# Kernel tuning notes

Hardware: AMD Instinct MI355X
Metric: run time of the kernel (lower is better)

## Reference

```python
import jax, jax.numpy as jnp
import numpy as np

D = 1024      # model dimension
H = 16        # heads
DK = D // H   # head dim
DFF = 4096    # ffn hidden
B, S = 2, 2048
EPS = 1e-6
NEG_SLOPE = 0.01  # torch LeakyReLU default


def setup_inputs() -> dict:
    key = jax.random.key(0)
    ks = jax.random.split(key, 12)
    sd = 1.0 / np.sqrt(D)
    sf = 1.0 / np.sqrt(DFF)
    return {
        "x": jax.random.normal(ks[0], (B, S, D), dtype=jnp.float32),
        "wq": jax.random.uniform(ks[1], (D, D), jnp.float32, -sd, sd),
        "bq": jnp.zeros((D,), jnp.float32),
        "wk": jax.random.uniform(ks[2], (D, D), jnp.float32, -sd, sd),
        "bk": jnp.zeros((D,), jnp.float32),
        "wv": jax.random.uniform(ks[3], (D, D), jnp.float32, -sd, sd),
        "bv": jnp.zeros((D,), jnp.float32),
        "wo": jax.random.uniform(ks[4], (D, D), jnp.float32, -sd, sd),
        "bo": jnp.zeros((D,), jnp.float32),
        "g1": jnp.ones((D,), jnp.float32),
        "b1": jnp.zeros((D,), jnp.float32),
        "w_ff1": jax.random.uniform(ks[5], (D, DFF), jnp.float32, -sd, sd),
        "b_ff1": jnp.zeros((DFF,), jnp.float32),
        "w_ff2": jax.random.uniform(ks[6], (DFF, D), jnp.float32, -sf, sf),
        "b_ff2": jnp.zeros((D,), jnp.float32),
        "g2": jnp.ones((D,), jnp.float32),
        "b2": jnp.zeros((D,), jnp.float32),
    }


def _layernorm(x, g, b):
    mu = jnp.mean(x, axis=-1, keepdims=True)
    var = jnp.mean(jnp.square(x - mu), axis=-1, keepdims=True)
    return (x - mu) * jax.lax.rsqrt(var + EPS) * g + b


def reference(x, wq, bq, wk, bk, wv, bv, wo, bo, g1, b1,
              w_ff1, b_ff1, w_ff2, b_ff2, g2, b2):
    # Multi-head attention
    q = (x @ wq + bq).reshape(B, S, H, DK).transpose(0, 2, 1, 3)  # [B,H,S,DK]
    k = (x @ wk + bk).reshape(B, S, H, DK).transpose(0, 2, 1, 3)
    v = (x @ wv + bv).reshape(B, S, H, DK).transpose(0, 2, 1, 3)
    scores = jnp.einsum('bhqd,bhkd->bhqk', q, k) / np.sqrt(DK)
    attn = jax.nn.softmax(scores, axis=-1)
    ctx = jnp.einsum('bhqk,bhkd->bhqd', attn, v)
    ctx = ctx.transpose(0, 2, 1, 3).reshape(B, S, D)
    attn_out = ctx @ wo + bo
    # residual + LN1 (dropout = identity in eval)
    h = _layernorm(attn_out + x, g1, b1)
    # FFN with LeakyReLU
    ff = jnp.where(h @ w_ff1 + b_ff1 > 0,
                   h @ w_ff1 + b_ff1,
                   NEG_SLOPE * (h @ w_ff1 + b_ff1))
    ff = ff @ w_ff2 + b_ff2
    return _layernorm(ff + h, g2, b2)
```

## Files before the change

### kernel.cpp

```cpp
#include <hip/hip_runtime.h>
#include <math.h>

#define D_MODEL 1024
#define NHEAD   16
#define DKH     64
#define DFF_    4096
#define BB      2
#define SS      2048
#define MTOT    (BB*SS)
#define EPSLN   1e-6f
#define NEG_SLOPE 0.01f

typedef unsigned short u16;
typedef unsigned int   u32;
typedef __bf16 bf16x8 __attribute__((ext_vector_type(8)));
typedef float  f32x4  __attribute__((ext_vector_type(4)));
typedef u16    u16x4  __attribute__((ext_vector_type(4)));

__device__ __forceinline__ u16 f2bf(float f) {
    u32 u = __float_as_uint(f);
    u = (u + 0x7fffu + ((u >> 16) & 1u)) >> 16;
    return (u16)u;
}
__device__ __forceinline__ float bf2f(u16 u) {
    return __uint_as_float(((u32)u) << 16);
}

__device__ __forceinline__ void gload_lds16(const u16* g, u16* l) {
    __builtin_amdgcn_global_load_lds(
        (const __attribute__((address_space(1))) u32*)g,
        (__attribute__((address_space(3))) u32*)l,
        16, 0, 0);
}

__device__ __forceinline__ void transpose_tile(const float* __restrict__ W,
        u16* __restrict__ WT, int N, int out_stride, int out_row_off,
        float scale, int bx, int by, u16* T)
{
    const int t  = threadIdx.x;
    const int n0 = bx * 64;
    const int k0 = by * 64;
    #pragma unroll
    for (int i = 0; i < 4; ++i) {
        int r = i * 16 + (t >> 4);
        int c = (t & 15) * 4;
        float4 v = *(const float4*)&W[(size_t)(k0 + r) * N + n0 + c];
        T[(c + 0) * 72 + r] = f2bf(v.x * scale);
        T[(c + 1) * 72 + r] = f2bf(v.y * scale);
        T[(c + 2) * 72 + r] = f2bf(v.z * scale);
        T[(c + 3) * 72 + r] = f2bf(v.w * scale);
    }
    __syncthreads();
    #pragma unroll
    for (int i = 0; i < 4; ++i) {
        int nr = i * 16 + (t >> 4);
        int kc = (t & 15) * 4;
        u16x4 o = { T[nr*72 + kc], T[nr*72 + kc + 1], T[nr*72 + kc + 2], T[nr*72 + kc + 3] };
        *(u16x4*)&WT[(size_t)(out_row_off + n0 + nr) * out_stride + k0 + kc] = o;
    }
}

__global__ __launch_bounds__(256)
void prep(const float* __restrict__ x, u16* __restrict__ x_bf,
          const float* __restrict__ wq, const float* __restrict__ wk,
          const float* __restrict__ wv, const float* __restrict__ wo,
          const float* __restrict__ wff1, const float* __restrict__ wff2,
          u16* __restrict__ wqkvT, u16* __restrict__ woT,
          u16* __restrict__ wff1T, u16* __restrict__ wff2T,
          const float* __restrict__ bq, const float* __restrict__ bk,
          const float* __restrict__ bv, float* __restrict__ qkv_bias,
          float qscale)
{
    __shared__ u16 T[64 * 72];
    int blk = blockIdx.x;
    if (blk < 4096) {
        int i = blk * 256 + threadIdx.x;
        float4 v = ((const float4*)x)[i];
        u16x4 o = { f2bf(v.x), f2bf(v.y), f2bf(v.z), f2bf(v.w) };
        ((u16x4*)x_bf)[i] = o;
        return;
    }
    blk -= 4096;
    if (blk < 1024) {
        int which = blk >> 8, r = blk & 255;
        const float* Ws = which == 0 ? wq : which == 1 ? wk : which == 2 ? wv : wo;
        u16* Wd   = which == 3 ? woT : wqkvT;
        int off   = which == 3 ? 0 : which * 1024;
        float sc  = which == 0 ? qscale : 1.0f;
        transpose_tile(Ws, Wd, 1024, 1024, off, sc, r & 15, r >> 4, T);
        return;
    }
    blk -= 1024;
    if (blk < 1024) {
        transpose_tile(wff1, wff1T, 4096, 1024, 0, 1.0f, blk & 63, blk >> 6, T);
        return;
    }
    blk -= 1024;
    if (blk < 1024) {
        transpose_tile(wff2, wff2T, 1024, 4096, 0, 1.0f, blk & 15, blk >> 4, T);
        return;
    }
    blk -= 1024;
    int i = blk * 256 + threadIdx.x;
    qkv_bias[i] = (i < 1024) ? bq[i] * qscale
                : (i < 2048) ? bk[i - 1024] : bv[i - 2048];
}

template<int EPI>
__global__ __launch_bounds__(256)
void gemm_bf16(const u16* __restrict__ A, const u16* __restrict__ BT,
               const float* __restrict__ bias, void* __restrict__ Cout,
               u16* __restrict__ Vt, int M, int N, int k_len, int kstride)
{
    __shared__ u16 As[128 * 64];
    __shared__ u16 Bs[128 * 64];
    const int tid  = threadIdx.x;
    const int w    = tid >> 6;
    const int lane = tid & 63;
    const int lm   = lane & 15;
    const int lq   = lane >> 4;
    const int nf = gridDim.x * gridDim.y;
    int f = blockIdx.y * gridDim.x + blockIdx.x;
    f = (f & 7) * (nf >> 3) + (f >> 3);
    const int row0 = (f / gridDim.x) * 128;
    const int col0 = (f % gridDim.x) * 128;
    const int k_off = blockIdx.z * k_len;
    const int wrow = (w >> 1) * 64;
    const int wcol = (w & 1) * 64;

    f32x4 acc[4][4] = {};

    const int r_i = lane >> 3;
    const int csw = ((lane & 7) ^ r_i) * 8;
    const u16* a_src = A  + (size_t)(row0 + w * 32 + r_i) * kstride + k_off + csw;
    const u16* b_src = BT + (size_t)(col0 + w * 32 + r_i) * kstride + k_off + csw;
    u16* a_dst = &As[(w * 32) * 64];
    u16* b_dst = &Bs[(w * 32) * 64];

    const int fr0 = (lq ^ (lm & 7)) * 8;
    const int fr1 = ((4 + lq) ^ (lm & 7)) * 8;
    const u16* a_rd = &As[(wrow + lm) * 64];
    const u16* b_rd = &Bs[(wcol + lm) * 64];

    for (int k0 = 0; k0 < k_len; k0 += 64) {
        #pragma unroll
        for (int i = 0; i < 4; ++i) {
            gload_lds16(a_src + k0 + (size_t)(i * 8) * kstride, a_dst + (i * 8) * 64);
            gload_lds16(b_src + k0 + (size_t)(i * 8) * kstride, b_dst + (i * 8) * 64);
        }
        __syncthreads();
        #pragma unroll
        for (int h = 0; h < 2; ++h) {
            const int fo = h ? fr1 : fr0;
            bf16x8 av[4], bv[4];
            #pragma unroll
            for (int m = 0; m < 4; ++m) av[m] = *(const bf16x8*)(a_rd + m * 16 * 64 + fo);
            #pragma unroll
            for (int n = 0; n < 4; ++n) bv[n] = *(const bf16x8*)(b_rd + n * 16 * 64 + fo);
            #pragma unroll
            for (int m = 0; m < 4; ++m)
                #pragma unroll
                for (int n = 0; n < 4; ++n)
                    acc[m][n] = __builtin_amdgcn_mfma_f32_16x16x32_bf16(av[m], bv[n], acc[m][n], 0, 0, 0);
        }
        __syncthreads();
    }

    float bz[4] = {0.f, 0.f, 0.f, 0.f};
    if (EPI != 3) {
        #pragma unroll
        for (int n = 0; n < 4; ++n) bz[n] = bias[col0 + wcol + n * 16 + lm];
    }

    if (EPI == 4 && col0 >= 2048) {
        #pragma unroll
        for (int m = 0; m < 4; ++m) {
            int rbase = row0 + wrow + m * 16 + lq * 4;
            int b = rbase >> 11, s = rbase & 2047;
            #pragma unroll
            for (int n = 0; n < 4; ++n) {
                int c = col0 + wcol + n * 16 + lm - 2048;
                u16x4 pk = { f2bf(acc[m][n][0] + bz[n]), f2bf(acc[m][n][1] + bz[n]),
                             f2bf(acc[m][n][2] + bz[n]), f2bf(acc[m][n][3] + bz[n]) };
                *(u16x4*)&Vt[(size_t)((b * 16 + (c >> 6)) * 64 + (c & 63)) * 2048 + s] = pk;
            }
        }
        return;
    }

    u16* Cz = (u16*)Cout + (EPI == 3 ? (size_t)blockIdx.z * M * N : 0);
    #pragma unroll
    for (int m = 0; m < 4; ++m) {
        #pragma unroll
        for (int e = 0; e < 4; ++e) {
            int row = row0 + wrow + m * 16 + lq * 4 + e;
            #pragma unroll
            for (int n = 0; n < 4; ++n) {
                int col = col0 + wcol + n * 16 + lm;
                float v = acc[m][n][e] + bz[n];
                if (EPI == 1) v = v > 0.f ? v : NEG_SLOPE * v;
                Cz[(size_t)row * N + col] = f2bf(v);
            }
        }
    }
}

__global__ __launch_bounds__(256, 4)
void attn_mfma(const u16* __restrict__ QKV, const u16* __restrict__ Vt,
               u16* __restrict__ ctx)
{
    __shared__ u16 QP[64 * 64];
    __shared__ u16 Kb[2][64 * 64];
    __shared__ u16 Vb[2][64 * 64];
    const int tid = threadIdx.x, w = tid >> 6, lane = tid & 63;
    const int lm = lane & 15, lq = lane >> 4;
    const int qh = w >> 1;
    const int kh = w & 1;
    int f = blockIdx.y * 32 + blockIdx.x;
    f = (f & 7) * 128 + (f >> 3);
    const int q0 = (f & 31) * 64;
    const int bh = f >> 5;
    const int b  = bh >> 4, h = bh & 15;
    const size_t row_b = (size_t)b * SS;
    const int ccol = h * DKH;

    const int r_i = lane >> 3;
    const int csw = ((lane & 7) ^ r_i) * 8;
    const u16* ksrc = QKV + (row_b + w * 16 + r_i) * 3072 + 1024 + ccol + csw;
    const u16* vsrc = Vt + ((size_t)bh * 64 + w * 16 + r_i) * SS + csw;
    const u16* qsrc = QKV + (row_b + q0 + w * 16 + r_i) * 3072 + ccol + csw;

    gload_lds16(qsrc,                    &QP[(w * 16) * 64]);
    gload_lds16(qsrc + (size_t)8 * 3072, &QP[(w * 16 + 8) * 64]);
    #pragma unroll
    for (int i = 0; i < 2; ++i) {
        gload_lds16(ksrc + (size_t)(i * 8) * 3072, &Kb[0][(w * 16 + i * 8) * 64]);
        gload_lds16(vsrc + (size_t)(i * 8) * SS,   &Vb[0][(w * 16 + i * 8) * 64]);
    }
    __syncthreads();

    const int fr0 = (lq ^ (lm & 7)) * 8;
    const int fr1 = ((4 + lq) ^ (lm & 7)) * 8;
    const int frp = kh ? fr1 : fr0;

    bf16x8 aq[2][2];
    #pragma unroll
    for (int m = 0; m < 2; ++m) {
        aq[m][0] = *(const bf16x8*)&QP[(qh * 32 + m * 16 + lm) * 64 + fr0];
        aq[m][1] = *(const bf16x8*)&QP[(qh * 32 + m * 16 + lm) * 64 + fr1];
    }
    __syncthreads();

    bf16x8 ones;
    #pragma unroll
    for (int j = 0; j < 8; ++j) ones[j] = (__bf16)1.0f;

    f32x4 o[2][4] = {};
    f32x4 lacc[2] = {};

    for (int kt = 0; kt < SS / 64; ++kt) {
        const int cur = kt & 1;
        if (kt < SS / 64 - 1) {
            const int nxt = cur ^ 1;
            const size_t koff = (size_t)(kt + 1) * 64;
            #pragma unroll
            for (int i = 0; i < 2; ++i) {
                gload_lds16(ksrc + (koff + i * 8) * 3072, &Kb[nxt][(w * 16 + i * 8) * 64]);
                gload_lds16(vsrc + koff + (size_t)(i * 8) * SS, &Vb[nxt][(w * 16 + i * 8) * 64]);
            }
        }
        f32x4 s[2][2] = {};
        #pragma unroll
        for (int n = 0; n < 2; ++n) {
            bf16x8 bk0 = *(const bf16x8*)&Kb[cur][(kh * 32 + n * 16 + lm) * 64 + fr0];
            bf16x8 bk1 = *(const bf16x8*)&Kb[cur][(kh * 32 + n * 16 + lm) * 64 + fr1];
            #pragma unroll
            for (int m = 0; m < 2; ++m) {
                s[m][n] = __builtin_amdgcn_mfma_f32_16x16x32_bf16(aq[m][0], bk0, s[m][n], 0, 0, 0);
                s[m][n] = __builtin_amdgcn_mfma_f32_16x16x32_bf16(aq[m][1], bk1, s[m][n], 0, 0, 0);
            }
        }
        const int rb = lq * 4;
        const int cw = lm & 7;
        #pragma unroll
        for (int m = 0; m < 2; ++m) {
            #pragma unroll
            for (int n = 0; n < 2; ++n) {
                const int cb = kh * 4 + n * 2 + (lm >> 3);
                #pragma unroll
                for (int e = 0; e < 4; ++e) {
                    float p = __builtin_exp2f(s[m][n][e]);
                    const int row = qh * 32 + m * 16 + rb + e;
                    QP[row * 64 + ((cb ^ ((rb + e) & 7)) * 8) + cw] =
                        (u16)((__float_as_uint(p) + 0x8000u) >> 16);
                }
            }
        }
        bf16x8 ap[2];
        #pragma unroll
        for (int m = 0; m < 2; ++m)
            ap[m] = *(const bf16x8*)&QP[(qh * 32 + m * 16 + lm) * 64 + frp];
        #pragma unroll
        for (int n = 0; n < 4; ++n) {
            bf16x8 bv = *(const bf16x8*)&Vb[cur][(n * 16 + lm) * 64 + frp];
            #pragma unroll
            for (int m = 0; m < 2; ++m)
                o[m][n] = __builtin_amdgcn_mfma_f32_16x16x32_bf16(ap[m], bv, o[m][n], 0, 0, 0);
        }
        #pragma unroll
        for (int m = 0; m < 2; ++m)
            lacc[m] = __builtin_amdgcn_mfma_f32_16x16x32_bf16(ap[m], ones, lacc[m], 0, 0, 0);
        __syncthreads();
    }

    if (kh == 1) {
        float* red = (float*)(qh == 0 ? (void*)Kb : (void*)Vb);
        #pragma unroll
        for (int m = 0; m < 2; ++m) {
            #pragma unroll
            for (int n = 0; n < 4; ++n)
                #pragma unroll
                for (int e = 0; e < 4; ++e)
                    red[((m * 4 + n) * 4 + e) * 64 + lane] = o[m][n][e];
            #pragma unroll
            for (int e = 0; e < 4; ++e)
                red[(32 + m * 4 + e) * 64 + lane] = lacc[m][e];
        }
    }
    __syncthreads();
    if (kh == 0) {
        const float* red = (const float*)(qh == 0 ? (void*)Kb : (void*)Vb);
        #pragma unroll
        for (int m = 0; m < 2; ++m) {
            #pragma unroll
            for (int e = 0; e < 4; ++e)
                lacc[m][e] += red[(32 + m * 4 + e) * 64 + lane];
            #pragma unroll
            for (int e = 0; e < 4; ++e) {
                float inv = 1.0f / lacc[m][e];
                int row = q0 + qh * 32 + m * 16 + lq * 4 + e;
                u16* dst = ctx + (row_b + row) * D_MODEL + ccol;
                #pragma unroll
                for (int n = 0; n < 4; ++n) {
                    float v = o[m][n][e] + red[((m * 4 + n) * 4 + e) * 64 + lane];
                    dst[n * 16 + lm] = f2bf(v * inv);
                }
            }
        }
    }
}

template<int OUTF32, int RESBF>
__global__ __launch_bounds__(256)
void add_ln(const u16* __restrict__ C0, const u16* __restrict__ C1,
            const float* __restrict__ cbias, const void* __restrict__ resid,
            const float* __restrict__ g, const float* __restrict__ beta,
            float* __restrict__ outf, u16* __restrict__ outb)
{
    __shared__ float red[8];
    const int row = blockIdx.x;
    const int tid = threadIdx.x;
    u16x4 p0 = ((const u16x4*)(C0 + (size_t)row * D_MODEL))[tid];
    u16x4 p1 = ((const u16x4*)(C1 + (size_t)row * D_MODEL))[tid];
    float4 cb = ((const float4*)cbias)[tid];
    float4 rr;
    if (RESBF) {
        u16x4 rb = ((const u16x4*)((const u16*)resid + (size_t)row * D_MODEL))[tid];
        rr = { bf2f(rb.x), bf2f(rb.y), bf2f(rb.z), bf2f(rb.w) };
    } else {
        rr = ((const float4*)((const float*)resid + (size_t)row * D_MODEL))[tid];
    }
    float4 v = { bf2f(p0.x) + bf2f(p1.x) + cb.x + rr.x,
                 bf2f(p0.y) + bf2f(p1.y) + cb.y + rr.y,
                 bf2f(p0.z) + bf2f(p1.z) + cb.z + rr.z,
                 bf2f(p0.w) + bf2f(p1.w) + cb.w + rr.w };
    float s  = v.x + v.y + v.z + v.w;
    float sq = v.x*v.x + v.y*v.y + v.z*v.z + v.w*v.w;
    #pragma unroll
    for (int off = 32; off > 0; off >>= 1) {
        s  += __shfl_down(s,  off, 64);
        sq += __shfl_down(sq, off, 64);
    }
    const int wv = tid >> 6;
    if ((tid & 63) == 0) { red[wv] = s; red[4 + wv] = sq; }
    __syncthreads();
    float st  = red[0] + red[1] + red[2] + red[3];
    float sqt = red[4] + red[5] + red[6] + red[7];
    float mu   = st * (1.0f / D_MODEL);
    float var  = sqt * (1.0f / D_MODEL) - mu * mu;
    float rstd = rsqrtf(var + EPSLN);
    float4 gv = ((const float4*)g)[tid];
    float4 bt = ((const float4*)beta)[tid];
    float4 ov;
    ov.x = (v.x - mu) * rstd * gv.x + bt.x;
    ov.y = (v.y - mu) * rstd * gv.y + bt.y;
    ov.z = (v.z - mu) * rstd * gv.z + bt.z;
    ov.w = (v.w - mu) * rstd * gv.w + bt.w;
    if (OUTF32) {
        ((float4*)(outf + (size_t)row * D_MODEL))[tid] = ov;
    } else {
        u16x4 ob = { f2bf(ov.x), f2bf(ov.y), f2bf(ov.z), f2bf(ov.w) };
        ((u16x4*)(outb + (size_t)row * D_MODEL))[tid] = ob;
    }
}

extern "C" void kernel_launch(void* const* d_in, const int* in_sizes, int n_in,
                              void* d_out, int out_size, void* d_ws, size_t ws_size,
                              hipStream_t stream) {
    const float* x     = (const float*)d_in[0];
    const float* wq    = (const float*)d_in[1];
    const float* bq    = (const float*)d_in[2];
    const float* wk    = (const float*)d_in[3];
    const float* bk    = (const float*)d_in[4];
    const float* wv    = (const float*)d_in[5];
    const float* bv    = (const float*)d_in[6];
    const float* wo    = (const float*)d_in[7];
    const float* bo    = (const float*)d_in[8];
    const float* g1    = (const float*)d_in[9];
    const float* b1    = (const float*)d_in[10];
    const float* w_ff1 = (const float*)d_in[11];
    const float* b_ff1 = (const float*)d_in[12];
    const float* w_ff2 = (const float*)d_in[13];
    const float* b_ff2 = (const float*)d_in[14];
    const float* g2    = (const float*)d_in[15];
    const float* b2    = (const float*)d_in[16];
    float* out = (float*)d_out;

    const float qscale = 0.18033688011112042f;

    char* W = (char*)d_ws;
    u16*   x_bf    = (u16*)(W + 0);
    u16*   wqkvT   = (u16*)(W + 8388608);
    u16*   woT     = (u16*)(W + 14680064);
    u16*   wff1T   = (u16*)(W + 16777216);
    u16*   wff2T   = (u16*)(W + 25165824);
    u16*   QKV     = (u16*)(W + 33554432);
    u16*   VtG     = (u16*)(W + 58720256);
    u16*   C0      = (u16*)(W + 67108864);
    u16*   C1      = (u16*)(W + 75497472);
    u16*   h_bf    = (u16*)(W + 83886080);
    float* qkv_bias= (float*)(W + 92274688);
    u16*   ctx     = x_bf;
    u16*   ff1_bf  = QKV;

    dim3 blk(256);
    prep<<<7180, blk, 0, stream>>>(x, x_bf, wq, wk, wv, wo, w_ff1, w_ff2,
                                   wqkvT, woT, wff1T, wff2T,
                                   bq, bk, bv, qkv_bias, qscale);
    gemm_bf16<4><<<dim3(24, 32, 1), blk, 0, stream>>>(x_bf, wqkvT, qkv_bias, QKV, VtG, MTOT, 3072, 1024, 1024);
    attn_mfma<<<dim3(32, 32), blk, 0, stream>>>(QKV, VtG, ctx);
    gemm_bf16<3><<<dim3(8, 32, 2), blk, 0, stream>>>(ctx, woT, nullptr, C0, nullptr, MTOT, 1024, 512, 1024);
    add_ln<0, 0><<<MTOT, blk, 0, stream>>>(C0, C1, bo, x, g1, b1, nullptr, h_bf);
    gemm_bf16<1><<<dim3(32, 32, 1), blk, 0, stream>>>(h_bf, wff1T, b_ff1, ff1_bf, nullptr, MTOT, DFF_, 1024, 1024);
    gemm_bf16<3><<<dim3(8, 32, 2), blk, 0, stream>>>(ff1_bf, wff2T, nullptr, C0, nullptr, MTOT, 1024, 2048, 4096);
    add_ln<1, 1><<<MTOT, blk, 0, stream>>>(C0, C1, b_ff2, h_bf, g2, b2, out, nullptr);
}
```

Measured before the change: 357.3 us.

## Add 256x256-tile 512-thread GEMM kernel for QKV and FFN1 projections

Adds a new GEMM kernel with 256x256 output tiles, 8 waves per block, double-buffered LDS with direct global-to-LDS loads interleaved between MFMA phases, and a grouped block-index swizzle for L2 locality. It replaces the 128-tile GEMM for the QKV and first FFN projections. The aim is more reuse per loaded operand and better overlap of loads with compute. The cost is 128KB of LDS per block and a large accumulator register footprint. The QKV grid of 192 blocks may leave some of the 256 CUs idle.

Measured after the change: 350.8 us. Within noise of the previous version (-1.8%).

```diff
diff --git a/kernel.cpp b/kernel.cpp
--- a/kernel.cpp
+++ b/kernel.cpp
@@ -172,14 +172,132 @@
         for (int n = 0; n < 4; ++n) bz[n] = bias[col0 + wcol + n * 16 + lm];
     }
 
+    u16* Cz = (u16*)Cout + (EPI == 3 ? (size_t)blockIdx.z * M * N : 0);
+    #pragma unroll
+    for (int m = 0; m < 4; ++m) {
+        #pragma unroll
+        for (int e = 0; e < 4; ++e) {
+            int row = row0 + wrow + m * 16 + lq * 4 + e;
+            #pragma unroll
+            for (int n = 0; n < 4; ++n) {
+                int col = col0 + wcol + n * 16 + lm;
+                float v = acc[m][n][e] + bz[n];
+                if (EPI == 1) v = v > 0.f ? v : NEG_SLOPE * v;
+                Cz[(size_t)row * N + col] = f2bf(v);
+            }
+        }
+    }
+}
+
+#define GPHASE(p) { \
+    bf16x8 a0h0 = *(const bf16x8*)&ar[(wm * 128 + (p) * 32 + lm) * 64 + fr0]; \
+    bf16x8 a0h1 = *(const bf16x8*)&ar[(wm * 128 + (p) * 32 + lm) * 64 + fr1]; \
+    bf16x8 a1h0 = *(const bf16x8*)&ar[(wm * 128 + (p) * 32 + 16 + lm) * 64 + fr0]; \
+    bf16x8 a1h1 = *(const bf16x8*)&ar[(wm * 128 + (p) * 32 + 16 + lm) * 64 + fr1]; \
+    _Pragma("unroll") \
+    for (int n = 0; n < 4; ++n) { \
+        acc[2*(p)][n]   = __builtin_amdgcn_mfma_f32_16x16x32_bf16(a0h0, bvf[n][0], acc[2*(p)][n], 0, 0, 0); \
+        acc[2*(p)][n]   = __builtin_amdgcn_mfma_f32_16x16x32_bf16(a0h1, bvf[n][1], acc[2*(p)][n], 0, 0, 0); \
+        acc[2*(p)+1][n] = __builtin_amdgcn_mfma_f32_16x16x32_bf16(a1h0, bvf[n][0], acc[2*(p)+1][n], 0, 0, 0); \
+        acc[2*(p)+1][n] = __builtin_amdgcn_mfma_f32_16x16x32_bf16(a1h1, bvf[n][1], acc[2*(p)+1][n], 0, 0, 0); \
+    } }
+
+template<int EPI>
+__global__ __launch_bounds__(512, 2)
+void gemm256(const u16* __restrict__ A, const u16* __restrict__ BT,
+             const float* __restrict__ bias, void* __restrict__ Cout,
+             u16* __restrict__ Vt, int M, int N, int k_len, int kstride)
+{
+    __shared__ u16 AS[2][256 * 64];
+    __shared__ u16 BS[2][256 * 64];
+    const int tid  = threadIdx.x;
+    const int w    = tid >> 6;
+    const int lane = tid & 63;
+    const int lm   = lane & 15;
+    const int lq   = lane >> 4;
+    const int wm   = w >> 2;
+    const int wn   = w & 3;
+
+    const int gx = gridDim.x;
+    const int nf = gx * gridDim.y;
+    int f = blockIdx.y * gx + blockIdx.x;
+    f = (f & 7) * (nf >> 3) + (f >> 3);
+    const int row0 = (f / gx) * 256;
+    const int col0 = (f % gx) * 256;
+
+    const int r_i = lane >> 3;
+    const int csw = ((lane & 7) ^ r_i) * 8;
+    const u16* a_src = A  + (size_t)(row0 + w * 8 + r_i) * kstride + csw;
+    const u16* b_src = BT + (size_t)(col0 + w * 8 + r_i) * kstride + csw;
+
+    const int fr0 = (lq ^ (lm & 7)) * 8;
+    const int fr1 = ((4 + lq) ^ (lm & 7)) * 8;
+
+    f32x4 acc[8][4] = {};
+    const int NT = k_len >> 6;
+
+    #pragma unroll
+    for (int j = 0; j < 4; ++j) {
+        gload_lds16(a_src + (size_t)(j * 64) * kstride, &AS[0][(j * 64 + w * 8) * 64]);
+        gload_lds16(b_src + (size_t)(j * 64) * kstride, &BS[0][(j * 64 + w * 8) * 64]);
+    }
+    __syncthreads();
+
+    for (int kt = 0; kt < NT; ++kt) {
+        const int cb = kt & 1, nb = cb ^ 1;
+        const bool pre = (kt + 1) < NT;
+        const u16* ar = &AS[cb][0];
+        const u16* br = &BS[cb][0];
+        u16* aw = &AS[nb][0];
+        u16* bw = &BS[nb][0];
+        const size_t knext = (size_t)(kt + 1) * 64;
+
+        if (pre) {
+            #pragma unroll
+            for (int j = 0; j < 4; ++j)
+                gload_lds16(b_src + (size_t)(j * 64) * kstride + knext,
+                            bw + (j * 64 + w * 8) * 64);
+            asm volatile("s_waitcnt vmcnt(6)" ::: "memory");
+        } else {
+            asm volatile("s_waitcnt vmcnt(2)" ::: "memory");
+        }
+        bf16x8 bvf[4][2];
+        #pragma unroll
+        for (int n = 0; n < 4; ++n) {
+            bvf[n][0] = *(const bf16x8*)&br[(wn * 64 + n * 16 + lm) * 64 + fr0];
+            bvf[n][1] = *(const bf16x8*)&br[(wn * 64 + n * 16 + lm) * 64 + fr1];
+        }
+        GPHASE(0)
+        if (pre) {
+            gload_lds16(a_src + knext,                                 aw + (w * 8) * 64);
+            gload_lds16(a_src + (size_t)128 * kstride + knext,         aw + (128 + w * 8) * 64);
+        }
+        GPHASE(1)
+        if (pre) {
+            gload_lds16(a_src + (size_t)64 * kstride + knext,          aw + (64 + w * 8) * 64);
+            gload_lds16(a_src + (size_t)192 * kstride + knext,         aw + (192 + w * 8) * 64);
+            asm volatile("s_waitcnt vmcnt(8)" ::: "memory");
+        } else {
+            asm volatile("s_waitcnt vmcnt(0)" ::: "memory");
+        }
+        GPHASE(2)
+        GPHASE(3)
+        asm volatile("" ::: "memory");
+        __builtin_amdgcn_s_barrier();
+    }
+
+    float bz[4];
+    #pragma unroll
+    for (int n = 0; n < 4; ++n) bz[n] = bias[col0 + wn * 64 + n * 16 + lm];
+
     if (EPI == 4 && col0 >= 2048) {
         #pragma unroll
-        for (int m = 0; m < 4; ++m) {
-            int rbase = row0 + wrow + m * 16 + lq * 4;
+        for (int m = 0; m < 8; ++m) {
+            int rbase = row0 + wm * 128 + m * 16 + lq * 4;
             int b = rbase >> 11, s = rbase & 2047;
             #pragma unroll
             for (int n = 0; n < 4; ++n) {
-                int c = col0 + wcol + n * 16 + lm - 2048;
+                int c = col0 + wn * 64 + n * 16 + lm - 2048;
                 u16x4 pk = { f2bf(acc[m][n][0] + bz[n]), f2bf(acc[m][n][1] + bz[n]),
                              f2bf(acc[m][n][2] + bz[n]), f2bf(acc[m][n][3] + bz[n]) };
                 *(u16x4*)&Vt[(size_t)((b * 16 + (c >> 6)) * 64 + (c & 63)) * 2048 + s] = pk;
@@ -188,15 +306,15 @@
         return;
     }
 
-    u16* Cz = (u16*)Cout + (EPI == 3 ? (size_t)blockIdx.z * M * N : 0);
-    #pragma unroll
-    for (int m = 0; m < 4; ++m) {
+    u16* Cz = (u16*)Cout;
+    #pragma unroll
+    for (int m = 0; m < 8; ++m) {
         #pragma unroll
         for (int e = 0; e < 4; ++e) {
-            int row = row0 + wrow + m * 16 + lq * 4 + e;
+            int row = row0 + wm * 128 + m * 16 + lq * 4 + e;
             #pragma unroll
             for (int n = 0; n < 4; ++n) {
-                int col = col0 + wcol + n * 16 + lm;
+                int col = col0 + wn * 64 + n * 16 + lm;
                 float v = acc[m][n][e] + bz[n];
                 if (EPI == 1) v = v > 0.f ? v : NEG_SLOPE * v;
                 Cz[(size_t)row * N + col] = f2bf(v);
@@ -444,14 +562,15 @@
     u16*   ff1_bf  = QKV;
 
     dim3 blk(256);
+    dim3 blk5(512);
     prep<<<7180, blk, 0, stream>>>(x, x_bf, wq, wk, wv, wo, w_ff1, w_ff2,
                                    wqkvT, woT, wff1T, wff2T,
                                    bq, bk, bv, qkv_bias, qscale);
-    gemm_bf16<4><<<dim3(24, 32, 1), blk, 0, stream>>>(x_bf, wqkvT, qkv_bias, QKV, VtG, MTOT, 3072, 1024, 1024);
+    gemm256<4><<<dim3(12, 16, 1), blk5, 0, stream>>>(x_bf, wqkvT, qkv_bias, QKV, VtG, MTOT, 3072, 1024, 1024);
     attn_mfma<<<dim3(32, 32), blk, 0, stream>>>(QKV, VtG, ctx);
     gemm_bf16<3><<<dim3(8, 32, 2), blk, 0, stream>>>(ctx, woT, nullptr, C0, nullptr, MTOT, 1024, 512, 1024);
     add_ln<0, 0><<<MTOT, blk, 0, stream>>>(C0, C1, bo, x, g1, b1, nullptr, h_bf);
-    gemm_bf16<1><<<dim3(32, 32, 1), blk, 0, stream>>>(h_bf, wff1T, b_ff1, ff1_bf, nullptr, MTOT, DFF_, 1024, 1024);
+    gemm256<1><<<dim3(16, 16, 1), blk5, 0, stream>>>(h_bf, wff1T, b_ff1, ff1_bf, nullptr, MTOT, DFF_, 1024, 1024);
     gemm_bf16<3><<<dim3(8, 32, 2), blk, 0, stream>>>(ff1_bf, wff2T, nullptr, C0, nullptr, MTOT, 1024, 2048, 4096);
     add_ln<1, 1><<<MTOT, blk, 0, stream>>>(C0, C1, b_ff2, h_bf, g2, b2, out, nullptr);
 }
```
